# Optimization experiments

Hardware: AMD Instinct MI355X
Metric: run time of the kernel (lower is better)

## Reference

```python
import jax, jax.numpy as jnp
import numpy as np


def conv2d(x, w, b, pad):
    # x: NCHW, w: OIHW, stride 1, symmetric padding
    y = jax.lax.conv_general_dilated(
        x, w, window_strides=(1, 1), padding=[(pad, pad), (pad, pad)],
        dimension_numbers=('NCHW', 'OIHW', 'NCHW'))
    return y + b[None, :, None, None]


def setup_inputs() -> dict:
    key = jax.random.key(0)
    ks = jax.random.split(key, 10)
    N, Cin, H, W = 8, 256, 64, 64
    Cr = 64
    wscale = 0.02  # keep softmax logits moderate
    return {
        'feature_maps': jax.random.normal(ks[0], (N, Cin, H, W), jnp.float32),
        'global_channel_output': jax.random.normal(ks[1], (N, Cin, H, W), jnp.float32),
        'wq': jax.random.normal(ks[2], (Cr, Cin, 3, 3), jnp.float32) * wscale,
        'bq': jnp.zeros((Cr,), jnp.float32),
        'wk': jax.random.normal(ks[3], (Cr, Cin, 5, 5), jnp.float32) * wscale,
        'bk': jnp.zeros((Cr,), jnp.float32),
        'wv': jax.random.normal(ks[4], (Cr, Cin, 7, 7), jnp.float32) * wscale,
        'bv': jnp.zeros((Cr,), jnp.float32),
        'watt': jax.random.normal(ks[5], (Cin, Cr, 1, 1), jnp.float32) * wscale,
        'batt': jnp.zeros((Cin,), jnp.float32),
    }


def reference(feature_maps, global_channel_output, wq, bq, wk, bk, wv, bv, watt, batt):
    N, Cin, H, W = feature_maps.shape
    HW = H * W
    q = conv2d(feature_maps, wq, bq, 1).reshape(N, -1, HW)  # (N, Cr, HW)
    k = conv2d(feature_maps, wk, bk, 2).reshape(N, -1, HW)
    v = conv2d(feature_maps, wv, bv, 3).reshape(N, -1, HW)
    # key^T @ query: (N, HW, HW)
    qk = jnp.einsum('nci,ncj->nij', k, q)
    # GLOBAL softmax over the whole flattened HW*HW matrix per sample
    qk = jax.nn.softmax(qk.reshape(N, -1), axis=-1).reshape(N, HW, HW)
    att = jnp.einsum('nci,nij->ncj', v, qk).reshape(N, -1, H, W)  # (N, Cr, H, W)
    att = conv2d(att, watt, batt, 0)  # (N, Cin, H, W)
    return global_channel_output * att + global_channel_output
```

## Files before the change

### kernel.cpp

```cpp
#include <hip/hip_runtime.h>
#include <math.h>

#define NB 8
#define CIN 256
#define CR 64
#define H 64
#define W 64
#define HW 4096

typedef _Float16 f16;
typedef _Float16 f16x8 __attribute__((ext_vector_type(8)));
typedef _Float16 f16x4 __attribute__((ext_vector_type(4)));
typedef float f32x4 __attribute__((ext_vector_type(4)));

static const size_t QKV = (size_t)NB * CR * HW;

__global__ __launch_bounds__(256) void prep_w(
    const float* __restrict__ src, f16* __restrict__ dst, int KK)
{
    int idx = blockIdx.x * 256 + threadIdx.x;
    int ci = idx & 255;
    int co = (idx >> 8) & 63;
    int off = idx >> 14;
    dst[((size_t)(off * 64 + co)) * 256 + ci] = (f16)src[((size_t)(co * 256 + ci)) * KK + off];
}

__global__ __launch_bounds__(256) void transpose_fm(
    const float* __restrict__ fm, f16* __restrict__ fmT)
{
    const int y = blockIdx.x & 63;
    const int n = blockIdx.x >> 6;
    const int tid = threadIdx.x;
    __shared__ f16x4 tile[64 * 64];
    const int xw = tid & 63;
    const int wv = tid >> 6;
    const float* s0 = fm + ((size_t)n * CIN) * HW + y * W + xw;
#pragma unroll
    for (int cc = 0; cc < 16; ++cc) {
        const int slot = wv * 16 + cc;
        const float* s = s0 + (size_t)(slot * 4) * HW;
        f16x4 pk;
#pragma unroll
        for (int e = 0; e < 4; ++e) pk[e] = (f16)s[(size_t)e * HW];
        tile[xw * 64 + (slot ^ xw)] = pk;
    }
    __syncthreads();
    f16x4* dst = (f16x4*)fmT + ((size_t)n * HW + y * W) * 64;
#pragma unroll
    for (int it = 0; it < 16; ++it) {
        const int idx = tid + it * 256;
        const int x = idx >> 6;
        const int slot = idx & 63;
        dst[x * 64 + slot] = tile[x * 64 + (slot ^ x)];
    }
}

template<int K, int LAYOUT>
__global__ __launch_bounds__(512) void conv_mfma(
    const f16* __restrict__ fmT, const f16* __restrict__ wT,
    const float* __restrict__ bias, f16* __restrict__ dst)
{
    constexpr int P = K / 2;
    constexpr int XBYTES = 2 * 72 * 128;
    constexpr int WBYTES = K * 64 * 128;
    constexpr int TBYTES = XBYTES + WBYTES;
    constexpr int SBYTES = (TBYTES > 32768) ? TBYTES : 32768;
    __shared__ __align__(16) unsigned char smem[SBYTES];
    unsigned char* Xl = smem;
    unsigned char* Wl = smem + XBYTES;

    const int bid0 = blockIdx.x;
    const int bid = (bid0 & 7) * 32 + (bid0 >> 3);
    const int n  = bid >> 5;
    const int y0 = (bid & 31) * 2;
    const int tid = threadIdx.x;
    const int w = tid >> 6;
    const int lane = tid & 63;
    const int r  = w >> 2;
    const int h  = (w >> 1) & 1;
    const int sw = w & 1;
    const int lm = lane & 15;
    const int g  = lane >> 4;

    if (tid < 128) {
        const int sl = tid >> 6;
        const int cidx = (tid >> 3) & 7;
        const int chunk = tid & 7;
        const int col = (cidx < P) ? cidx : (64 + cidx);
        *(uint4*)(Xl + (size_t)(sl * 72 + col) * 128 + chunk * 16) = uint4{0, 0, 0, 0};
    }

    f32x4 acc[2][4];
#pragma unroll
    for (int i = 0; i < 2; ++i)
#pragma unroll
        for (int j = 0; j < 4; ++j) acc[i][j] = f32x4{0.f, 0.f, 0.f, 0.f};

    for (int dy = 0; dy < K; ++dy) {
        for (int ch = 0; ch < 4; ++ch) {
            __syncthreads();
#pragma unroll
            for (int p = 0; p < 2; ++p) {
                const int idx = tid + p * 512;
                const int sl = idx >> 9;
                const int x = (idx >> 3) & 63;
                const int chunk = idx & 7;
                const int iy = y0 + sl + dy - P;
                uint4 val = uint4{0, 0, 0, 0};
                if (iy >= 0 && iy < H)
                    val = *(const uint4*)(fmT + ((size_t)n * HW + iy * 64 + x) * 256 +
                                          ch * 64 + chunk * 8);
                *(uint4*)(Xl + (size_t)(sl * 72 + x + P) * 128 +
                          ((chunk * 16) ^ (((x + P) & 7) << 4))) = val;
            }
#pragma unroll
            for (int p = 0; p < K; ++p) {
                const int idx = tid + p * 512;
                const int cig = idx & 7;
                const int co  = (idx >> 3) & 63;
                const int dx  = idx >> 9;
                const f16* s = wT + ((size_t)((dy * K + dx) * 64 + co)) * 256 + ch * 64 + cig * 8;
                *(uint4*)(Wl + (size_t)(dx * 64 + co) * 128 +
                          ((cig * 16) ^ ((co & 7) << 4))) = *(const uint4*)s;
            }
            __syncthreads();
#pragma unroll
            for (int dx = 0; dx < K; ++dx) {
                f16x8 a[2], b[4];
#pragma unroll
                for (int cf = 0; cf < 2; ++cf) {
                    const int co = h * 32 + cf * 16 + lm;
                    a[cf] = *(const f16x8*)(Wl + (size_t)(dx * 64 + co) * 128 +
                                            ((sw * 64 + g * 16) ^ ((co & 7) << 4)));
                }
#pragma unroll
                for (int xf = 0; xf < 4; ++xf) {
                    const int col = xf * 16 + lm + dx;
                    b[xf] = *(const f16x8*)(Xl + (size_t)(r * 72 + col) * 128 +
                                            ((sw * 64 + g * 16) ^ ((col & 7) << 4)));
                }
#pragma unroll
                for (int cf = 0; cf < 2; ++cf)
#pragma unroll
                    for (int xf = 0; xf < 4; ++xf)
                        acc[cf][xf] = __builtin_amdgcn_mfma_f32_16x16x32_f16(
                            a[cf], b[xf], acc[cf][xf], 0, 0, 0);
            }
        }
    }

    __syncthreads();
    {
        const int mslot = r * 2 + h;
        if (sw == 1) {
#pragma unroll
            for (int cf = 0; cf < 2; ++cf)
#pragma unroll
                for (int xf = 0; xf < 4; ++xf)
                    *(f32x4*)(smem + (size_t)(mslot * 64 + lane) * 128 +
                              (((cf * 4 + xf) * 16) ^ ((lane & 7) << 4))) = acc[cf][xf];
        }
        __syncthreads();
        if (sw == 0) {
#pragma unroll
            for (int cf = 0; cf < 2; ++cf)
#pragma unroll
                for (int xf = 0; xf < 4; ++xf)
                    acc[cf][xf] += *(const f32x4*)(smem + (size_t)(mslot * 64 + lane) * 128 +
                                                   (((cf * 4 + xf) * 16) ^ ((lane & 7) << 4)));
        }
    }

    if (sw == 0) {
        const int y = y0 + r;
#pragma unroll
        for (int cf = 0; cf < 2; ++cf) {
            const float4 bv = *(const float4*)(bias + h * 32 + cf * 16 + g * 4);
            if (LAYOUT == 0) {
#pragma unroll
                for (int xf = 0; xf < 4; ++xf) {
                    f16x4 pk;
#pragma unroll
                    for (int e = 0; e < 4; ++e)
                        pk[e] = (f16)(acc[cf][xf][e] + ((const float*)&bv)[e]);
                    *(f16x4*)(dst + ((size_t)n * HW + y * W + xf * 16 + lm) * 64 +
                              h * 32 + cf * 16 + g * 4) = pk;
                }
            } else {
#pragma unroll
                for (int e = 0; e < 4; ++e) {
                    const int co = h * 32 + cf * 16 + g * 4 + e;
#pragma unroll
                    for (int xf = 0; xf < 4; ++xf)
                        dst[((size_t)(n * CR + co)) * HW + y * W + xf * 16 + lm] =
                            (f16)(acc[cf][xf][e] + ((const float*)&bv)[e]);
                }
            }
        }
    }
}

__global__ __launch_bounds__(256, 2) void attn_mfma(
    const f16* __restrict__ qT, const f16* __restrict__ kT, const f16* __restrict__ vv,
    f16* __restrict__ attu, float* __restrict__ Mcol, float* __restrict__ Zcol)
{
    const int bid0 = blockIdx.x;
    const int bid = (bid0 & 7) * 64 + (bid0 >> 3);
    const int jt = bid & 63;
    const int n  = bid >> 6;
    const int j0 = jt * 64;
    const int tid = threadIdx.x;
    const int wv = tid >> 6;
    const int lane = tid & 63;
    const int lm = lane & 15;
    const int g  = lane >> 4;
    const int key = (lm & 7) << 4;

    __shared__ __align__(16) f16 Qt[64 * 64];
    __shared__ __align__(16) f16 Kt[64 * 64];
    __shared__ __align__(16) f16 Vt[64 * 64];

    {
        const int r = tid >> 2;
        const f16* src = qT + ((size_t)n * HW + j0 + r) * 64;
#pragma unroll
        for (int h = 0; h < 2; ++h) {
            const int ch = (tid & 3) * 2 + h;
            *(uint4*)((char*)Qt + r * 128 + ((ch * 16) ^ ((r & 7) << 4))) =
                *(const uint4*)(src + ch * 8);
        }
    }

    float m = -1e30f, z = 0.f;
    f32x4 accp[4];
#pragma unroll
    for (int c = 0; c < 4; ++c) accp[c] = f32x4{0.f, 0.f, 0.f, 0.f};

    for (int it = 0; it < 64; ++it) {
        const int i0 = it * 64;
        __syncthreads();
        {
            const int r = tid >> 2;
            const f16* ks = kT + ((size_t)n * HW + i0 + r) * 64;
            const f16* vs = vv + ((size_t)n * CR + r) * HW + i0;
#pragma unroll
            for (int h = 0; h < 2; ++h) {
                const int ch = (tid & 3) * 2 + h;
                *(uint4*)((char*)Kt + r * 128 + ((ch * 16) ^ ((r & 7) << 4))) =
                    *(const uint4*)(ks + ch * 8);
                *(uint4*)((char*)Vt + r * 128 + ((ch * 16) ^ ((r & 7) << 4))) =
                    *(const uint4*)(vs + ch * 8);
            }
        }
        __syncthreads();

        f32x4 sacc[4];
#pragma unroll
        for (int f = 0; f < 4; ++f) sacc[f] = f32x4{0.f, 0.f, 0.f, 0.f};
#pragma unroll
        for (int ks = 0; ks < 2; ++ks) {
            const int off = (ks * 64 + g * 16);
            const f16x8 B = *(const f16x8*)((char*)Qt + (wv * 16 + lm) * 128 + (off ^ key));
#pragma unroll
            for (int f = 0; f < 4; ++f) {
                const f16x8 A = *(const f16x8*)((char*)Kt + (f * 16 + lm) * 128 + (off ^ key));
                sacc[f] = __builtin_amdgcn_mfma_f32_16x16x32_f16(A, B, sacc[f], 0, 0, 0);
            }
        }

        float mt = -1e30f;
#pragma unroll
        for (int f = 0; f < 4; ++f)
#pragma unroll
            for (int e = 0; e < 4; ++e) mt = fmaxf(mt, sacc[f][e]);
        mt = fmaxf(mt, __shfl_xor(mt, 16));
        mt = fmaxf(mt, __shfl_xor(mt, 32));
        const float mnew = fmaxf(m, mt);
        const float rr = __expf(m - mnew);
        m = mnew;

        f16x4 p16[4];
        float zt = 0.f;
#pragma unroll
        for (int f = 0; f < 4; ++f) {
#pragma unroll
            for (int e = 0; e < 4; ++e) {
                const float ev = __expf(sacc[f][e] - mnew);
                zt += ev;
                p16[f][e] = (f16)ev;
            }
        }
        zt += __shfl_xor(zt, 16);
        zt += __shfl_xor(zt, 32);
        z = z * rr + zt;

#pragma unroll
        for (int cf = 0; cf < 4; ++cf) {
            accp[cf][0] *= rr; accp[cf][1] *= rr;
            accp[cf][2] *= rr; accp[cf][3] *= rr;
        }

#pragma unroll
        for (int cf = 0; cf < 4; ++cf) {
#pragma unroll
            for (int f = 0; f < 4; ++f) {
                const f16x4 A = *(const f16x4*)((char*)Vt + (cf * 16 + lm) * 128 +
                                                ((f * 32 + g * 8) ^ key));
                accp[cf] = __builtin_amdgcn_mfma_f32_16x16x16f16(A, p16[f], accp[cf], 0, 0, 0);
            }
        }
    }

    const int j = j0 + wv * 16 + lm;
    const size_t jbase = ((size_t)n * HW + j) * 64;
#pragma unroll
    for (int cf = 0; cf < 4; ++cf) {
        f16x4 pk;
#pragma unroll
        for (int e = 0; e < 4; ++e) pk[e] = (f16)accp[cf][e];
        *(f16x4*)(attu + jbase + cf * 16 + g * 4) = pk;
    }
    if (g == 0) {
        Mcol[(size_t)n * HW + j] = m;
        Zcol[(size_t)n * HW + j] = z;
    }
}

__global__ __launch_bounds__(256) void reduce_kernel(
    const float* __restrict__ Mcol, const float* __restrict__ Zcol,
    float* __restrict__ Mn, float* __restrict__ Zn)
{
    const int n = blockIdx.x;
    const int tid = threadIdx.x;
    __shared__ float red[256];

    float lm = -1e30f;
    for (int j = tid; j < HW; j += 256) lm = fmaxf(lm, Mcol[(size_t)n * HW + j]);
    red[tid] = lm; __syncthreads();
    for (int s = 128; s > 0; s >>= 1) {
        if (tid < s) red[tid] = fmaxf(red[tid], red[tid + s]);
        __syncthreads();
    }
    const float M = red[0];
    __syncthreads();

    float ls = 0.f;
    for (int j = tid; j < HW; j += 256)
        ls += Zcol[(size_t)n * HW + j] * __expf(Mcol[(size_t)n * HW + j] - M);
    red[tid] = ls; __syncthreads();
    for (int s = 128; s > 0; s >>= 1) {
        if (tid < s) red[tid] += red[tid + s];
        __syncthreads();
    }
    if (tid == 0) { Mn[n] = M; Zn[n] = red[0]; }
}

__global__ __launch_bounds__(512) void final_mfma(
    const f16* __restrict__ attu, const float* __restrict__ Mcol,
    const float* __restrict__ Mn, const float* __restrict__ Zn,
    const float* __restrict__ watt, const float* __restrict__ batt,
    const float* __restrict__ gco, float* __restrict__ out)
{
    __shared__ __align__(16) f16 Wl[256 * 64];
    __shared__ __align__(16) f16 Al[128 * 64];

    const int bid0 = blockIdx.x;
    const int bid = (bid0 & 7) * 32 + (bid0 >> 3);
    const int n  = bid >> 5;
    const int p0 = (bid & 31) * 128;
    const int tid = threadIdx.x;
    const int wv = tid >> 6;
    const int lane = tid & 63;
    const int lm = lane & 15;
    const int g  = lane >> 4;

#pragma unroll
    for (int t = 0; t < 8; ++t) {
        const int idx = tid + t * 512;
        const int co = idx >> 4;
        const int ch = idx & 15;
        const float4 w4 = *(const float4*)(watt + (size_t)co * 64 + ch * 4);
        f16x4 pk;
        pk[0] = (f16)w4.x; pk[1] = (f16)w4.y; pk[2] = (f16)w4.z; pk[3] = (f16)w4.w;
        *(f16x4*)((char*)Wl + co * 128 + ((ch * 8) ^ ((co & 7) << 4))) = pk;
    }
#pragma unroll
    for (int t = 0; t < 4; ++t) {
        const int idx = tid + t * 512;
        const int pp = idx >> 3;
        const int ch = idx & 7;
        *(uint4*)((char*)Al + pp * 128 + ((ch * 16) ^ ((pp & 7) << 4))) =
            *(const uint4*)(attu + ((size_t)n * HW + p0 + pp) * 64 + ch * 8);
    }
    __syncthreads();

    f32x4 acc[2][8];
#pragma unroll
    for (int cf = 0; cf < 2; ++cf)
#pragma unroll
        for (int pf = 0; pf < 8; ++pf) acc[cf][pf] = f32x4{0.f, 0.f, 0.f, 0.f};

#pragma unroll
    for (int ks = 0; ks < 2; ++ks) {
        const int off = ks * 64 + g * 16;
        f16x8 A[2], B[8];
#pragma unroll
        for (int cf = 0; cf < 2; ++cf) {
            const int co = wv * 32 + cf * 16 + lm;
            A[cf] = *(const f16x8*)((char*)Wl + co * 128 + (off ^ ((co & 7) << 4)));
        }
#pragma unroll
        for (int pf = 0; pf < 8; ++pf) {
            const int pp = pf * 16 + lm;
            B[pf] = *(const f16x8*)((char*)Al + pp * 128 + (off ^ ((pp & 7) << 4)));
        }
#pragma unroll
        for (int cf = 0; cf < 2; ++cf)
#pragma unroll
            for (int pf = 0; pf < 8; ++pf)
                acc[cf][pf] = __builtin_amdgcn_mfma_f32_16x16x32_f16(
                    A[cf], B[pf], acc[cf][pf], 0, 0, 0);
    }

    const float M = Mn[n];
    const float Zi = 1.f / Zn[n];
    float ecol[8];
#pragma unroll
    for (int pf = 0; pf < 8; ++pf)
        ecol[pf] = __expf(Mcol[(size_t)n * HW + p0 + pf * 16 + lm] - M) * Zi;

#pragma unroll
    for (int cf = 0; cf < 2; ++cf) {
#pragma unroll
        for (int e = 0; e < 4; ++e) {
            const int co = wv * 32 + cf * 16 + g * 4 + e;
            const float bb = batt[co] + 1.f;
            const float* gsrc = gco + (size_t)(n * CIN + co) * HW + p0 + lm;
            float* dstp = out + (size_t)(n * CIN + co) * HW + p0 + lm;
#pragma unroll
            for (int pf = 0; pf < 8; ++pf) {
                const float gvv = gsrc[pf * 16];
                dstp[pf * 16] = gvv * (acc[cf][pf][e] * ecol[pf] + bb);
            }
        }
    }
}

extern "C" void kernel_launch(void* const* d_in, const int* in_sizes, int n_in,
                              void* d_out, int out_size, void* d_ws, size_t ws_size,
                              hipStream_t stream)
{
    (void)in_sizes; (void)n_in; (void)out_size; (void)ws_size;
    const float* fm   = (const float*)d_in[0];
    const float* gco  = (const float*)d_in[1];
    const float* wq   = (const float*)d_in[2];
    const float* bq   = (const float*)d_in[3];
    const float* wk   = (const float*)d_in[4];
    const float* bk   = (const float*)d_in[5];
    const float* wv   = (const float*)d_in[6];
    const float* bv   = (const float*)d_in[7];
    const float* watt = (const float*)d_in[8];
    const float* batt = (const float*)d_in[9];
    float* out = (float*)d_out;

    f16* qT   = (f16*)out;
    f16* kT   = qT + QKV;
    f16* vvb  = kT + QKV;
    f16* fmT  = vvb + QKV;

    unsigned char* wsb = (unsigned char*)d_ws;
    f16* wTq = (f16*)(wsb);
    f16* wTk = (f16*)(wsb + 294912);
    f16* wTv = (f16*)(wsb + 1114112);
    f16* attu = (f16*)(wsb + 2719744);
    float* Mcol = (float*)(wsb + 6914048);
    float* Zcol = (float*)(wsb + 7045120);
    float* Mn   = (float*)(wsb + 7176192);
    float* Zn   = (float*)(wsb + 7176224);

    prep_w<<<576, 256, 0, stream>>>(wq, wTq, 9);
    prep_w<<<1600, 256, 0, stream>>>(wk, wTk, 25);
    prep_w<<<3136, 256, 0, stream>>>(wv, wTv, 49);
    transpose_fm<<<NB * 64, 256, 0, stream>>>(fm, fmT);

    conv_mfma<3, 0><<<256, 512, 0, stream>>>(fmT, wTq, bq, qT);
    conv_mfma<5, 0><<<256, 512, 0, stream>>>(fmT, wTk, bk, kT);
    conv_mfma<7, 1><<<256, 512, 0, stream>>>(fmT, wTv, bv, vvb);

    attn_mfma<<<NB * 64, 256, 0, stream>>>(qT, kT, vvb, attu, Mcol, Zcol);
    reduce_kernel<<<NB, 256, 0, stream>>>(Mcol, Zcol, Mn, Zn);
    final_mfma<<<256, 512, 0, stream>>>(attu, Mcol, Mn, Zn, watt, batt, gco, out);
}
```

Baseline: 227.8 us.

## Rewrite attention kernel with 32x32 MFMA, register-resident Q, async LDS double buffering

```diff
diff --git a/kernel.cpp b/kernel.cpp
--- a/kernel.cpp
+++ b/kernel.cpp
@@ -12,8 +12,28 @@
 typedef _Float16 f16x8 __attribute__((ext_vector_type(8)));
 typedef _Float16 f16x4 __attribute__((ext_vector_type(4)));
 typedef float f32x4 __attribute__((ext_vector_type(4)));
+typedef float f32x16 __attribute__((ext_vector_type(16)));
+typedef unsigned int u32;
+typedef unsigned int u32x4 __attribute__((ext_vector_type(4)));
 
 static const size_t QKV = (size_t)NB * CR * HW;
+
+static __device__ __forceinline__ void gl_lds16(const f16* g, f16* l) {
+    __builtin_amdgcn_global_load_lds(
+        (const __attribute__((address_space(1))) void*)g,
+        (__attribute__((address_space(3))) void*)l, 16, 0, 0);
+}
+
+static __device__ __forceinline__ u32 pk2(float a, float b) {
+    return __builtin_bit_cast(u32, __builtin_amdgcn_cvt_pkrtz(a, b));
+}
+
+static __device__ __forceinline__ f32x16 zero16() {
+    f32x16 v;
+#pragma unroll
+    for (int i = 0; i < 16; ++i) v[i] = 0.f;
+    return v;
+}
 
 __global__ __launch_bounds__(256) void prep_w(
     const float* __restrict__ src, f16* __restrict__ dst, int KK)
@@ -58,7 +78,7 @@
 template<int K, int LAYOUT>
 __global__ __launch_bounds__(512) void conv_mfma(
     const f16* __restrict__ fmT, const f16* __restrict__ wT,
-    const float* __restrict__ bias, f16* __restrict__ dst)
+    const float* __restrict__ bias, f16* __restrict__ dst, float oscale)
 {
     constexpr int P = K / 2;
     constexpr int XBYTES = 2 * 72 * 128;
@@ -182,7 +202,7 @@
                     f16x4 pk;
 #pragma unroll
                     for (int e = 0; e < 4; ++e)
-                        pk[e] = (f16)(acc[cf][xf][e] + ((const float*)&bv)[e]);
+                        pk[e] = (f16)((acc[cf][xf][e] + ((const float*)&bv)[e]) * oscale);
                     *(f16x4*)(dst + ((size_t)n * HW + y * W + xf * 16 + lm) * 64 +
                               h * 32 + cf * 16 + g * 4) = pk;
                 }
@@ -193,134 +213,159 @@
 #pragma unroll
                     for (int xf = 0; xf < 4; ++xf)
                         dst[((size_t)(n * CR + co)) * HW + y * W + xf * 16 + lm] =
-                            (f16)(acc[cf][xf][e] + ((const float*)&bv)[e]);
+                            (f16)((acc[cf][xf][e] + ((const float*)&bv)[e]) * oscale);
                 }
             }
         }
     }
 }
 
-__global__ __launch_bounds__(256, 2) void attn_mfma(
+__global__ __launch_bounds__(256, 1) void attn_mfma(
     const f16* __restrict__ qT, const f16* __restrict__ kT, const f16* __restrict__ vv,
     f16* __restrict__ attu, float* __restrict__ Mcol, float* __restrict__ Zcol)
 {
     const int bid0 = blockIdx.x;
-    const int bid = (bid0 & 7) * 64 + (bid0 >> 3);
-    const int jt = bid & 63;
-    const int n  = bid >> 6;
-    const int j0 = jt * 64;
+    const int bid = (bid0 & 7) * 32 + (bid0 >> 3);
+    const int n  = bid >> 5;
+    const int jb = bid & 31;
     const int tid = threadIdx.x;
     const int wv = tid >> 6;
     const int lane = tid & 63;
-    const int lm = lane & 15;
-    const int g  = lane >> 4;
-    const int key = (lm & 7) << 4;
-
-    __shared__ __align__(16) f16 Qt[64 * 64];
-    __shared__ __align__(16) f16 Kt[64 * 64];
-    __shared__ __align__(16) f16 Vt[64 * 64];
-
+    const int lm5 = lane & 31;
+    const int g1 = lane >> 5;
+    const int j = jb * 128 + wv * 32 + lm5;
+    const int key = (lm5 & 7) << 4;
+
+    __shared__ __align__(16) f16 KV[2][2][64 * 64];
+
+    const int rsub = lane >> 3;
+    const int perm = ((lane & 7) ^ rsub) << 3;
+    const f16* kS = kT + ((size_t)n * HW) * 64;
+    const f16* vS = vv + ((size_t)n * CR) * HW;
+
+    f16x8 qf[4];
     {
-        const int r = tid >> 2;
-        const f16* src = qT + ((size_t)n * HW + j0 + r) * 64;
-#pragma unroll
-        for (int h = 0; h < 2; ++h) {
-            const int ch = (tid & 3) * 2 + h;
-            *(uint4*)((char*)Qt + r * 128 + ((ch * 16) ^ ((r & 7) << 4))) =
-                *(const uint4*)(src + ch * 8);
-        }
+        const f16* qp = qT + ((size_t)n * HW + j) * 64 + g1 * 8;
+#pragma unroll
+        for (int ks = 0; ks < 4; ++ks) qf[ks] = *(const f16x8*)(qp + ks * 16);
     }
 
     float m = -1e30f, z = 0.f;
-    f32x4 accp[4];
-#pragma unroll
-    for (int c = 0; c < 4; ++c) accp[c] = f32x4{0.f, 0.f, 0.f, 0.f};
-
+    f32x16 acc0 = zero16(), acc1 = zero16();
+
+#pragma unroll
+    for (int h = 0; h < 2; ++h) {
+        const int q = 2 * wv + h;
+        gl_lds16(kS + (size_t)(q * 8 + rsub) * 64 + perm, &KV[0][0][q * 512]);
+        gl_lds16(vS + (size_t)(q * 8 + rsub) * HW + perm, &KV[0][1][q * 512]);
+    }
+    __syncthreads();
+
+    int buf = 0;
     for (int it = 0; it < 64; ++it) {
-        const int i0 = it * 64;
-        __syncthreads();
-        {
-            const int r = tid >> 2;
-            const f16* ks = kT + ((size_t)n * HW + i0 + r) * 64;
-            const f16* vs = vv + ((size_t)n * CR + r) * HW + i0;
+        const char* Kb = (const char*)&KV[buf][0][0];
+        f32x16 s0 = zero16(), s1 = zero16();
+        __builtin_amdgcn_s_setprio(1);
+#pragma unroll
+        for (int ks = 0; ks < 4; ++ks) {
+            const int off = ((ks * 32 + g1 * 16) ^ key);
+            const f16x8 A0 = *(const f16x8*)(Kb + lm5 * 128 + off);
+            const f16x8 A1 = *(const f16x8*)(Kb + (32 + lm5) * 128 + off);
+            s0 = __builtin_amdgcn_mfma_f32_32x32x16_f16(A0, qf[ks], s0, 0, 0, 0);
+            s1 = __builtin_amdgcn_mfma_f32_32x32x16_f16(A1, qf[ks], s1, 0, 0, 0);
+        }
+        __builtin_amdgcn_s_setprio(0);
+
+        if (it < 63) {
 #pragma unroll
             for (int h = 0; h < 2; ++h) {
-                const int ch = (tid & 3) * 2 + h;
-                *(uint4*)((char*)Kt + r * 128 + ((ch * 16) ^ ((r & 7) << 4))) =
-                    *(const uint4*)(ks + ch * 8);
-                *(uint4*)((char*)Vt + r * 128 + ((ch * 16) ^ ((r & 7) << 4))) =
-                    *(const uint4*)(vs + ch * 8);
-            }
-        }
-        __syncthreads();
-
-        f32x4 sacc[4];
-#pragma unroll
-        for (int f = 0; f < 4; ++f) sacc[f] = f32x4{0.f, 0.f, 0.f, 0.f};
-#pragma unroll
-        for (int ks = 0; ks < 2; ++ks) {
-            const int off = (ks * 64 + g * 16);
-            const f16x8 B = *(const f16x8*)((char*)Qt + (wv * 16 + lm) * 128 + (off ^ key));
-#pragma unroll
-            for (int f = 0; f < 4; ++f) {
-                const f16x8 A = *(const f16x8*)((char*)Kt + (f * 16 + lm) * 128 + (off ^ key));
-                sacc[f] = __builtin_amdgcn_mfma_f32_16x16x32_f16(A, B, sacc[f], 0, 0, 0);
-            }
-        }
-
-        float mt = -1e30f;
-#pragma unroll
-        for (int f = 0; f < 4; ++f)
-#pragma unroll
-            for (int e = 0; e < 4; ++e) mt = fmaxf(mt, sacc[f][e]);
-        mt = fmaxf(mt, __shfl_xor(mt, 16));
+                const int q = 2 * wv + h;
+                gl_lds16(kS + (size_t)((it + 1) * 64 + q * 8 + rsub) * 64 + perm,
+                         &KV[buf ^ 1][0][q * 512]);
+                gl_lds16(vS + (size_t)(q * 8 + rsub) * HW + (it + 1) * 64 + perm,
+                         &KV[buf ^ 1][1][q * 512]);
+            }
+        }
+
+        float mt = s0[0];
+#pragma unroll
+        for (int rr2 = 1; rr2 < 16; ++rr2) mt = fmaxf(mt, s0[rr2]);
+#pragma unroll
+        for (int rr2 = 0; rr2 < 16; ++rr2) mt = fmaxf(mt, s1[rr2]);
         mt = fmaxf(mt, __shfl_xor(mt, 32));
-        const float mnew = fmaxf(m, mt);
-        const float rr = __expf(m - mnew);
-        m = mnew;
-
-        f16x4 p16[4];
+        if (__ballot(mt > m)) {
+            const float mnew = fmaxf(m, mt);
+            const float rsc = exp2f(m - mnew);
+            z *= rsc;
+#pragma unroll
+            for (int rr2 = 0; rr2 < 16; ++rr2) { acc0[rr2] *= rsc; acc1[rr2] *= rsc; }
+            m = mnew;
+        }
         float zt = 0.f;
-#pragma unroll
-        for (int f = 0; f < 4; ++f) {
-#pragma unroll
-            for (int e = 0; e < 4; ++e) {
-                const float ev = __expf(sacc[f][e] - mnew);
-                zt += ev;
-                p16[f][e] = (f16)ev;
-            }
-        }
-        zt += __shfl_xor(zt, 16);
+        u32 pa0[8], pa1[8];
+#pragma unroll
+        for (int a = 0; a < 4; ++a) {
+            float p0 = exp2f(s0[4 * a + 0] - m), p1 = exp2f(s0[4 * a + 1] - m);
+            float p2 = exp2f(s0[4 * a + 2] - m), p3 = exp2f(s0[4 * a + 3] - m);
+            zt += (p0 + p1) + (p2 + p3);
+            pa0[a * 2 + 0] = pk2(p0, p1); pa0[a * 2 + 1] = pk2(p2, p3);
+            float q0 = exp2f(s1[4 * a + 0] - m), q1 = exp2f(s1[4 * a + 1] - m);
+            float q2 = exp2f(s1[4 * a + 2] - m), q3 = exp2f(s1[4 * a + 3] - m);
+            zt += (q0 + q1) + (q2 + q3);
+            pa1[a * 2 + 0] = pk2(q0, q1); pa1[a * 2 + 1] = pk2(q2, q3);
+        }
         zt += __shfl_xor(zt, 32);
-        z = z * rr + zt;
-
-#pragma unroll
-        for (int cf = 0; cf < 4; ++cf) {
-            accp[cf][0] *= rr; accp[cf][1] *= rr;
-            accp[cf][2] *= rr; accp[cf][3] *= rr;
-        }
-
-#pragma unroll
-        for (int cf = 0; cf < 4; ++cf) {
-#pragma unroll
-            for (int f = 0; f < 4; ++f) {
-                const f16x4 A = *(const f16x4*)((char*)Vt + (cf * 16 + lm) * 128 +
-                                                ((f * 32 + g * 8) ^ key));
-                accp[cf] = __builtin_amdgcn_mfma_f32_16x16x16f16(A, p16[f], accp[cf], 0, 0, 0);
-            }
-        }
-    }
-
-    const int j = j0 + wv * 16 + lm;
+        z += zt;
+
+        u32 bfu[4][4];
+#pragma unroll
+        for (int it2 = 0; it2 < 2; ++it2) {
+            const u32* P = (it2 == 0) ? pa0 : pa1;
+#pragma unroll
+            for (int k2 = 0; k2 < 2; ++k2) {
+                const u32 sA = g1 ? P[(k2 * 2 + 0) * 2 + 0] : P[(k2 * 2 + 1) * 2 + 0];
+                const u32 sB = g1 ? P[(k2 * 2 + 0) * 2 + 1] : P[(k2 * 2 + 1) * 2 + 1];
+                const u32 rA = __shfl_xor(sA, 32);
+                const u32 rB = __shfl_xor(sB, 32);
+                const u32 oA = g1 ? P[(k2 * 2 + 1) * 2 + 0] : P[(k2 * 2 + 0) * 2 + 0];
+                const u32 oB = g1 ? P[(k2 * 2 + 1) * 2 + 1] : P[(k2 * 2 + 0) * 2 + 1];
+                bfu[it2 * 2 + k2][0] = g1 ? rA : oA;
+                bfu[it2 * 2 + k2][1] = g1 ? rB : oB;
+                bfu[it2 * 2 + k2][2] = g1 ? oA : rA;
+                bfu[it2 * 2 + k2][3] = g1 ? oB : rB;
+            }
+        }
+
+        const char* Vb = (const char*)&KV[buf][1][0];
+        __builtin_amdgcn_s_setprio(1);
+#pragma unroll
+        for (int ks2 = 0; ks2 < 4; ++ks2) {
+            const f16x8 B = __builtin_bit_cast(
+                f16x8, (u32x4){bfu[ks2][0], bfu[ks2][1], bfu[ks2][2], bfu[ks2][3]});
+            const int off = ((ks2 * 32 + g1 * 16) ^ key);
+            const f16x8 A0 = *(const f16x8*)(Vb + lm5 * 128 + off);
+            const f16x8 A1 = *(const f16x8*)(Vb + (32 + lm5) * 128 + off);
+            acc0 = __builtin_amdgcn_mfma_f32_32x32x16_f16(A0, B, acc0, 0, 0, 0);
+            acc1 = __builtin_amdgcn_mfma_f32_32x32x16_f16(A1, B, acc1, 0, 0, 0);
+        }
+        __builtin_amdgcn_s_setprio(0);
+
+        if (it < 63) {
+            __syncthreads();
+            buf ^= 1;
+        }
+    }
+
     const size_t jbase = ((size_t)n * HW + j) * 64;
 #pragma unroll
-    for (int cf = 0; cf < 4; ++cf) {
-        f16x4 pk;
-#pragma unroll
-        for (int e = 0; e < 4; ++e) pk[e] = (f16)accp[cf][e];
-        *(f16x4*)(attu + jbase + cf * 16 + g * 4) = pk;
-    }
-    if (g == 0) {
+    for (int a = 0; a < 4; ++a) {
+        f16x4 pk0, pk1;
+#pragma unroll
+        for (int e = 0; e < 4; ++e) { pk0[e] = (f16)acc0[4 * a + e]; pk1[e] = (f16)acc1[4 * a + e]; }
+        *(f16x4*)(attu + jbase + a * 8 + g1 * 4) = pk0;
+        *(f16x4*)(attu + jbase + 32 + a * 8 + g1 * 4) = pk1;
+    }
+    if (g1 == 0) {
         Mcol[(size_t)n * HW + j] = m;
         Zcol[(size_t)n * HW + j] = z;
     }
@@ -346,7 +391,7 @@
 
     float ls = 0.f;
     for (int j = tid; j < HW; j += 256)
-        ls += Zcol[(size_t)n * HW + j] * __expf(Mcol[(size_t)n * HW + j] - M);
+        ls += Zcol[(size_t)n * HW + j] * exp2f(Mcol[(size_t)n * HW + j] - M);
     red[tid] = ls; __syncthreads();
     for (int s = 128; s > 0; s >>= 1) {
         if (tid < s) red[tid] += red[tid + s];
@@ -427,7 +472,7 @@
     float ecol[8];
 #pragma unroll
     for (int pf = 0; pf < 8; ++pf)
-        ecol[pf] = __expf(Mcol[(size_t)n * HW + p0 + pf * 16 + lm] - M) * Zi;
+        ecol[pf] = exp2f(Mcol[(size_t)n * HW + p0 + pf * 16 + lm] - M) * Zi;
 
 #pragma unroll
     for (int cf = 0; cf < 2; ++cf) {
@@ -478,16 +523,18 @@
     float* Mn   = (float*)(wsb + 7176192);
     float* Zn   = (float*)(wsb + 7176224);
 
+    const float LOG2E = 1.4426950408889634f;
+
     prep_w<<<576, 256, 0, stream>>>(wq, wTq, 9);
     prep_w<<<1600, 256, 0, stream>>>(wk, wTk, 25);
     prep_w<<<3136, 256, 0, stream>>>(wv, wTv, 49);
     transpose_fm<<<NB * 64, 256, 0, stream>>>(fm, fmT);
 
-    conv_mfma<3, 0><<<256, 512, 0, stream>>>(fmT, wTq, bq, qT);
-    conv_mfma<5, 0><<<256, 512, 0, stream>>>(fmT, wTk, bk, kT);
-    conv_mfma<7, 1><<<256, 512, 0, stream>>>(fmT, wTv, bv, vvb);
-
-    attn_mfma<<<NB * 64, 256, 0, stream>>>(qT, kT, vvb, attu, Mcol, Zcol);
+    conv_mfma<3, 0><<<256, 512, 0, stream>>>(fmT, wTq, bq, qT, LOG2E);
+    conv_mfma<5, 0><<<256, 512, 0, stream>>>(fmT, wTk, bk, kT, 1.0f);
+    conv_mfma<7, 1><<<256, 512, 0, stream>>>(fmT, wTv, bv, vvb, 1.0f);
+
+    attn_mfma<<<256, 256, 0, stream>>>(qT, kT, vvb, attu, Mcol, Zcol);
     reduce_kernel<<<NB, 256, 0, stream>>>(Mcol, Zcol, Mn, Zn);
     final_mfma<<<256, 512, 0, stream>>>(attu, Mcol, Mn, Zn, watt, batt, gco, out);
 }
```

Measured after the change: 253.9 us. 11.5% more time.

## Double-buffer K/V via direct global-to-LDS loads and use exp2 with prescaled Q

Applied to the files above, without the earlier changes.

```diff
diff --git a/kernel.cpp b/kernel.cpp
--- a/kernel.cpp
+++ b/kernel.cpp
@@ -14,6 +14,12 @@
 typedef float f32x4 __attribute__((ext_vector_type(4)));
 
 static const size_t QKV = (size_t)NB * CR * HW;
+
+static __device__ __forceinline__ void gl_lds16(const f16* g, f16* l) {
+    __builtin_amdgcn_global_load_lds(
+        (const __attribute__((address_space(1))) void*)g,
+        (__attribute__((address_space(3))) void*)l, 16, 0, 0);
+}
 
 __global__ __launch_bounds__(256) void prep_w(
     const float* __restrict__ src, f16* __restrict__ dst, int KK)
@@ -58,7 +64,7 @@
 template<int K, int LAYOUT>
 __global__ __launch_bounds__(512) void conv_mfma(
     const f16* __restrict__ fmT, const f16* __restrict__ wT,
-    const float* __restrict__ bias, f16* __restrict__ dst)
+    const float* __restrict__ bias, f16* __restrict__ dst, float oscale)
 {
     constexpr int P = K / 2;
     constexpr int XBYTES = 2 * 72 * 128;
@@ -94,7 +100,7 @@
 #pragma unroll
     for (int i = 0; i < 2; ++i)
 #pragma unroll
-        for (int j = 0; j < 4; ++j) acc[i][j] = f32x4{0.f, 0.f, 0.f, 0.f};
+        for (int jx = 0; jx < 4; ++jx) acc[i][jx] = f32x4{0.f, 0.f, 0.f, 0.f};
 
     for (int dy = 0; dy < K; ++dy) {
         for (int ch = 0; ch < 4; ++ch) {
@@ -182,7 +188,7 @@
                     f16x4 pk;
 #pragma unroll
                     for (int e = 0; e < 4; ++e)
-                        pk[e] = (f16)(acc[cf][xf][e] + ((const float*)&bv)[e]);
+                        pk[e] = (f16)((acc[cf][xf][e] + ((const float*)&bv)[e]) * oscale);
                     *(f16x4*)(dst + ((size_t)n * HW + y * W + xf * 16 + lm) * 64 +
                               h * 32 + cf * 16 + g * 4) = pk;
                 }
@@ -193,7 +199,7 @@
 #pragma unroll
                     for (int xf = 0; xf < 4; ++xf)
                         dst[((size_t)(n * CR + co)) * HW + y * W + xf * 16 + lm] =
-                            (f16)(acc[cf][xf][e] + ((const float*)&bv)[e]);
+                            (f16)((acc[cf][xf][e] + ((const float*)&bv)[e]) * oscale);
                 }
             }
         }
@@ -215,20 +221,20 @@
     const int lm = lane & 15;
     const int g  = lane >> 4;
     const int key = (lm & 7) << 4;
-
-    __shared__ __align__(16) f16 Qt[64 * 64];
-    __shared__ __align__(16) f16 Kt[64 * 64];
-    __shared__ __align__(16) f16 Vt[64 * 64];
-
+    const int j = j0 + wv * 16 + lm;
+
+    __shared__ __align__(16) f16 KV[2][2][64 * 64];
+
+    const int rsub = lane >> 3;
+    const int perm = ((lane & 7) ^ rsub) << 3;
+    const f16* kS = kT + ((size_t)n * HW) * 64;
+    const f16* vS = vv + ((size_t)n * CR) * HW;
+
+    f16x8 qf[2];
     {
-        const int r = tid >> 2;
-        const f16* src = qT + ((size_t)n * HW + j0 + r) * 64;
-#pragma unroll
-        for (int h = 0; h < 2; ++h) {
-            const int ch = (tid & 3) * 2 + h;
-            *(uint4*)((char*)Qt + r * 128 + ((ch * 16) ^ ((r & 7) << 4))) =
-                *(const uint4*)(src + ch * 8);
-        }
+        const f16* qp = qT + ((size_t)n * HW + j) * 64 + g * 8;
+        qf[0] = *(const f16x8*)(qp);
+        qf[1] = *(const f16x8*)(qp + 32);
     }
 
     float m = -1e30f, z = 0.f;
@@ -236,82 +242,95 @@
 #pragma unroll
     for (int c = 0; c < 4; ++c) accp[c] = f32x4{0.f, 0.f, 0.f, 0.f};
 
+#pragma unroll
+    for (int h = 0; h < 2; ++h) {
+        const int q = 2 * wv + h;
+        gl_lds16(kS + (size_t)(q * 8 + rsub) * 64 + perm, &KV[0][0][q * 512]);
+        gl_lds16(vS + (size_t)(q * 8 + rsub) * HW + perm, &KV[0][1][q * 512]);
+    }
+    __syncthreads();
+
+    int buf = 0;
     for (int it = 0; it < 64; ++it) {
-        const int i0 = it * 64;
-        __syncthreads();
-        {
-            const int r = tid >> 2;
-            const f16* ks = kT + ((size_t)n * HW + i0 + r) * 64;
-            const f16* vs = vv + ((size_t)n * CR + r) * HW + i0;
+        if (it < 63) {
 #pragma unroll
             for (int h = 0; h < 2; ++h) {
-                const int ch = (tid & 3) * 2 + h;
-                *(uint4*)((char*)Kt + r * 128 + ((ch * 16) ^ ((r & 7) << 4))) =
-                    *(const uint4*)(ks + ch * 8);
-                *(uint4*)((char*)Vt + r * 128 + ((ch * 16) ^ ((r & 7) << 4))) =
-                    *(const uint4*)(vs + ch * 8);
-            }
-        }
-        __syncthreads();
-
+                const int q = 2 * wv + h;
+                gl_lds16(kS + (size_t)((it + 1) * 64 + q * 8 + rsub) * 64 + perm,
+                         &KV[buf ^ 1][0][q * 512]);
+                gl_lds16(vS + (size_t)(q * 8 + rsub) * HW + (it + 1) * 64 + perm,
+                         &KV[buf ^ 1][1][q * 512]);
+            }
+        }
+
+        const char* Kb = (const char*)&KV[buf][0][0];
         f32x4 sacc[4];
 #pragma unroll
         for (int f = 0; f < 4; ++f) sacc[f] = f32x4{0.f, 0.f, 0.f, 0.f};
+        __builtin_amdgcn_s_setprio(1);
 #pragma unroll
         for (int ks = 0; ks < 2; ++ks) {
-            const int off = (ks * 64 + g * 16);
-            const f16x8 B = *(const f16x8*)((char*)Qt + (wv * 16 + lm) * 128 + (off ^ key));
+            const int off = (ks * 64 + g * 16) ^ key;
 #pragma unroll
             for (int f = 0; f < 4; ++f) {
-                const f16x8 A = *(const f16x8*)((char*)Kt + (f * 16 + lm) * 128 + (off ^ key));
-                sacc[f] = __builtin_amdgcn_mfma_f32_16x16x32_f16(A, B, sacc[f], 0, 0, 0);
-            }
-        }
-
-        float mt = -1e30f;
+                const f16x8 A = *(const f16x8*)(Kb + (f * 16 + lm) * 128 + off);
+                sacc[f] = __builtin_amdgcn_mfma_f32_16x16x32_f16(A, qf[ks], sacc[f], 0, 0, 0);
+            }
+        }
+        __builtin_amdgcn_s_setprio(0);
+
+        float mt = sacc[0][0];
 #pragma unroll
         for (int f = 0; f < 4; ++f)
 #pragma unroll
             for (int e = 0; e < 4; ++e) mt = fmaxf(mt, sacc[f][e]);
         mt = fmaxf(mt, __shfl_xor(mt, 16));
         mt = fmaxf(mt, __shfl_xor(mt, 32));
-        const float mnew = fmaxf(m, mt);
-        const float rr = __expf(m - mnew);
-        m = mnew;
-
+        if (__ballot(mt > m)) {
+            const float mnew = fmaxf(m, mt);
+            const float rsc = exp2f(m - mnew);
+            z *= rsc;
+#pragma unroll
+            for (int cf = 0; cf < 4; ++cf) {
+                accp[cf][0] *= rsc; accp[cf][1] *= rsc;
+                accp[cf][2] *= rsc; accp[cf][3] *= rsc;
+            }
+            m = mnew;
+        }
         f16x4 p16[4];
         float zt = 0.f;
 #pragma unroll
         for (int f = 0; f < 4; ++f) {
 #pragma unroll
             for (int e = 0; e < 4; ++e) {
-                const float ev = __expf(sacc[f][e] - mnew);
+                const float ev = exp2f(sacc[f][e] - m);
                 zt += ev;
                 p16[f][e] = (f16)ev;
             }
         }
         zt += __shfl_xor(zt, 16);
         zt += __shfl_xor(zt, 32);
-        z = z * rr + zt;
-
+        z += zt;
+
+        const char* Vb = (const char*)&KV[buf][1][0];
+        __builtin_amdgcn_s_setprio(1);
 #pragma unroll
         for (int cf = 0; cf < 4; ++cf) {
-            accp[cf][0] *= rr; accp[cf][1] *= rr;
-            accp[cf][2] *= rr; accp[cf][3] *= rr;
-        }
-
-#pragma unroll
-        for (int cf = 0; cf < 4; ++cf) {
 #pragma unroll
             for (int f = 0; f < 4; ++f) {
-                const f16x4 A = *(const f16x4*)((char*)Vt + (cf * 16 + lm) * 128 +
+                const f16x4 A = *(const f16x4*)(Vb + (cf * 16 + lm) * 128 +
                                                 ((f * 32 + g * 8) ^ key));
                 accp[cf] = __builtin_amdgcn_mfma_f32_16x16x16f16(A, p16[f], accp[cf], 0, 0, 0);
             }
         }
-    }
-
-    const int j = j0 + wv * 16 + lm;
+        __builtin_amdgcn_s_setprio(0);
+
+        if (it < 63) {
+            __syncthreads();
+            buf ^= 1;
+        }
+    }
+
     const size_t jbase = ((size_t)n * HW + j) * 64;
 #pragma unroll
     for (int cf = 0; cf < 4; ++cf) {
@@ -346,7 +365,7 @@
 
     float ls = 0.f;
     for (int j = tid; j < HW; j += 256)
-        ls += Zcol[(size_t)n * HW + j] * __expf(Mcol[(size_t)n * HW + j] - M);
+        ls += Zcol[(size_t)n * HW + j] * exp2f(Mcol[(size_t)n * HW + j] - M);
     red[tid] = ls; __syncthreads();
     for (int s = 128; s > 0; s >>= 1) {
         if (tid < s) red[tid] += red[tid + s];
@@ -427,7 +446,7 @@
     float ecol[8];
 #pragma unroll
     for (int pf = 0; pf < 8; ++pf)
-        ecol[pf] = __expf(Mcol[(size_t)n * HW + p0 + pf * 16 + lm] - M) * Zi;
+        ecol[pf] = exp2f(Mcol[(size_t)n * HW + p0 + pf * 16 + lm] - M) * Zi;
 
 #pragma unroll
     for (int cf = 0; cf < 2; ++cf) {
@@ -478,14 +497,16 @@
     float* Mn   = (float*)(wsb + 7176192);
     float* Zn   = (float*)(wsb + 7176224);
 
+    const float LOG2E = 1.4426950408889634f;
+
     prep_w<<<576, 256, 0, stream>>>(wq, wTq, 9);
     prep_w<<<1600, 256, 0, stream>>>(wk, wTk, 25);
     prep_w<<<3136, 256, 0, stream>>>(wv, wTv, 49);
     transpose_fm<<<NB * 64, 256, 0, stream>>>(fm, fmT);
 
-    conv_mfma<3, 0><<<256, 512, 0, stream>>>(fmT, wTq, bq, qT);
-    conv_mfma<5, 0><<<256, 512, 0, stream>>>(fmT, wTk, bk, kT);
-    conv_mfma<7, 1><<<256, 512, 0, stream>>>(fmT, wTv, bv, vvb);
+    conv_mfma<3, 0><<<256, 512, 0, stream>>>(fmT, wTq, bq, qT, LOG2E);
+    conv_mfma<5, 0><<<256, 512, 0, stream>>>(fmT, wTk, bk, kT, 1.0f);
+    conv_mfma<7, 1><<<256, 512, 0, stream>>>(fmT, wTv, bv, vvb, 1.0f);
 
     attn_mfma<<<NB * 64, 256, 0, stream>>>(qT, kT, vvb, attu, Mcol, Zcol);
     reduce_kernel<<<NB, 256, 0, stream>>>(Mcol, Zcol, Mn, Zn);
```

Measured after the change: 239.6 us. 1.05x slower.

## Merge conv and weight-prep launches, fold log2e into Q, and skip unneeded rescales

Applied to the files above, without the earlier changes.

```diff
diff --git a/kernel.cpp b/kernel.cpp
--- a/kernel.cpp
+++ b/kernel.cpp
@@ -15,10 +15,21 @@
 
 static const size_t QKV = (size_t)NB * CR * HW;
 
-__global__ __launch_bounds__(256) void prep_w(
-    const float* __restrict__ src, f16* __restrict__ dst, int KK)
-{
-    int idx = blockIdx.x * 256 + threadIdx.x;
+static __device__ __forceinline__ float ex2(float x) {
+    return __builtin_amdgcn_exp2f(x);
+}
+
+__global__ __launch_bounds__(256) void prep_all(
+    const float* __restrict__ wq, const float* __restrict__ wk,
+    const float* __restrict__ wv,
+    f16* __restrict__ dq, f16* __restrict__ dk, f16* __restrict__ dv)
+{
+    int b = blockIdx.x;
+    const float* src; f16* dst; int KK;
+    if (b < 576)       { src = wq; dst = dq; KK = 9; }
+    else if (b < 2176) { src = wk; dst = dk; KK = 25; b -= 576; }
+    else               { src = wv; dst = dv; KK = 49; b -= 2176; }
+    int idx = b * 256 + threadIdx.x;
     int ci = idx & 255;
     int co = (idx >> 8) & 63;
     int off = idx >> 14;
@@ -56,20 +67,16 @@
 }
 
 template<int K, int LAYOUT>
-__global__ __launch_bounds__(512) void conv_mfma(
+static __device__ __forceinline__ void conv_body(
     const f16* __restrict__ fmT, const f16* __restrict__ wT,
-    const float* __restrict__ bias, f16* __restrict__ dst)
+    const float* __restrict__ bias, f16* __restrict__ dst, float oscale,
+    unsigned char* smem, int bid0)
 {
     constexpr int P = K / 2;
     constexpr int XBYTES = 2 * 72 * 128;
-    constexpr int WBYTES = K * 64 * 128;
-    constexpr int TBYTES = XBYTES + WBYTES;
-    constexpr int SBYTES = (TBYTES > 32768) ? TBYTES : 32768;
-    __shared__ __align__(16) unsigned char smem[SBYTES];
     unsigned char* Xl = smem;
     unsigned char* Wl = smem + XBYTES;
 
-    const int bid0 = blockIdx.x;
     const int bid = (bid0 & 7) * 32 + (bid0 >> 3);
     const int n  = bid >> 5;
     const int y0 = (bid & 31) * 2;
@@ -94,7 +101,7 @@
 #pragma unroll
     for (int i = 0; i < 2; ++i)
 #pragma unroll
-        for (int j = 0; j < 4; ++j) acc[i][j] = f32x4{0.f, 0.f, 0.f, 0.f};
+        for (int jx = 0; jx < 4; ++jx) acc[i][jx] = f32x4{0.f, 0.f, 0.f, 0.f};
 
     for (int dy = 0; dy < K; ++dy) {
         for (int ch = 0; ch < 4; ++ch) {
@@ -182,7 +189,7 @@
                     f16x4 pk;
 #pragma unroll
                     for (int e = 0; e < 4; ++e)
-                        pk[e] = (f16)(acc[cf][xf][e] + ((const float*)&bv)[e]);
+                        pk[e] = (f16)((acc[cf][xf][e] + ((const float*)&bv)[e]) * oscale);
                     *(f16x4*)(dst + ((size_t)n * HW + y * W + xf * 16 + lm) * 64 +
                               h * 32 + cf * 16 + g * 4) = pk;
                 }
@@ -193,11 +200,24 @@
 #pragma unroll
                     for (int xf = 0; xf < 4; ++xf)
                         dst[((size_t)(n * CR + co)) * HW + y * W + xf * 16 + lm] =
-                            (f16)(acc[cf][xf][e] + ((const float*)&bv)[e]);
+                            (f16)((acc[cf][xf][e] + ((const float*)&bv)[e]) * oscale);
                 }
             }
         }
     }
+}
+
+__global__ __launch_bounds__(512) void conv_all(
+    const f16* __restrict__ fmT,
+    const f16* __restrict__ wTq, const f16* __restrict__ wTk, const f16* __restrict__ wTv,
+    const float* __restrict__ bq, const float* __restrict__ bk, const float* __restrict__ bv,
+    f16* __restrict__ qT, f16* __restrict__ kT, f16* __restrict__ vvb, float log2e)
+{
+    __shared__ __align__(16) unsigned char smem[2 * 72 * 128 + 7 * 64 * 128];
+    const int b = blockIdx.x;
+    if (b < 256)      conv_body<3, 0>(fmT, wTq, bq, qT, log2e, smem, b);
+    else if (b < 512) conv_body<5, 0>(fmT, wTk, bk, kT, 1.0f, smem, b - 256);
+    else              conv_body<7, 1>(fmT, wTv, bv, vvb, 1.0f, smem, b - 512);
 }
 
 __global__ __launch_bounds__(256, 2) void attn_mfma(
@@ -258,8 +278,8 @@
 #pragma unroll
         for (int f = 0; f < 4; ++f) sacc[f] = f32x4{0.f, 0.f, 0.f, 0.f};
 #pragma unroll
-        for (int ks = 0; ks < 2; ++ks) {
-            const int off = (ks * 64 + g * 16);
+        for (int ks2 = 0; ks2 < 2; ++ks2) {
+            const int off = (ks2 * 64 + g * 16);
             const f16x8 B = *(const f16x8*)((char*)Qt + (wv * 16 + lm) * 128 + (off ^ key));
 #pragma unroll
             for (int f = 0; f < 4; ++f) {
@@ -268,37 +288,38 @@
             }
         }
 
-        float mt = -1e30f;
-#pragma unroll
-        for (int f = 0; f < 4; ++f)
-#pragma unroll
-            for (int e = 0; e < 4; ++e) mt = fmaxf(mt, sacc[f][e]);
+        const float mA = fmaxf(fmaxf(sacc[0][0], sacc[0][1]), fmaxf(sacc[0][2], sacc[0][3]));
+        const float mB = fmaxf(fmaxf(sacc[1][0], sacc[1][1]), fmaxf(sacc[1][2], sacc[1][3]));
+        const float mC = fmaxf(fmaxf(sacc[2][0], sacc[2][1]), fmaxf(sacc[2][2], sacc[2][3]));
+        const float mD = fmaxf(fmaxf(sacc[3][0], sacc[3][1]), fmaxf(sacc[3][2], sacc[3][3]));
+        float mt = fmaxf(fmaxf(mA, mB), fmaxf(mC, mD));
         mt = fmaxf(mt, __shfl_xor(mt, 16));
         mt = fmaxf(mt, __shfl_xor(mt, 32));
-        const float mnew = fmaxf(m, mt);
-        const float rr = __expf(m - mnew);
-        m = mnew;
-
+        if (__ballot(mt > m)) {
+            const float mnew = fmaxf(m, mt);
+            const float rsc = ex2(m - mnew);
+            z *= rsc;
+#pragma unroll
+            for (int cf = 0; cf < 4; ++cf) {
+                accp[cf][0] *= rsc; accp[cf][1] *= rsc;
+                accp[cf][2] *= rsc; accp[cf][3] *= rsc;
+            }
+            m = mnew;
+        }
         f16x4 p16[4];
-        float zt = 0.f;
+        float zp[4];
 #pragma unroll
         for (int f = 0; f < 4; ++f) {
-#pragma unroll
-            for (int e = 0; e < 4; ++e) {
-                const float ev = __expf(sacc[f][e] - mnew);
-                zt += ev;
-                p16[f][e] = (f16)ev;
-            }
-        }
+            const float e0 = ex2(sacc[f][0] - m), e1 = ex2(sacc[f][1] - m);
+            const float e2 = ex2(sacc[f][2] - m), e3 = ex2(sacc[f][3] - m);
+            zp[f] = (e0 + e1) + (e2 + e3);
+            p16[f][0] = (f16)e0; p16[f][1] = (f16)e1;
+            p16[f][2] = (f16)e2; p16[f][3] = (f16)e3;
+        }
+        float zt = (zp[0] + zp[1]) + (zp[2] + zp[3]);
         zt += __shfl_xor(zt, 16);
         zt += __shfl_xor(zt, 32);
-        z = z * rr + zt;
-
-#pragma unroll
-        for (int cf = 0; cf < 4; ++cf) {
-            accp[cf][0] *= rr; accp[cf][1] *= rr;
-            accp[cf][2] *= rr; accp[cf][3] *= rr;
-        }
+        z += zt;
 
 #pragma unroll
         for (int cf = 0; cf < 4; ++cf) {
@@ -346,7 +367,7 @@
 
     float ls = 0.f;
     for (int j = tid; j < HW; j += 256)
-        ls += Zcol[(size_t)n * HW + j] * __expf(Mcol[(size_t)n * HW + j] - M);
+        ls += Zcol[(size_t)n * HW + j] * ex2(Mcol[(size_t)n * HW + j] - M);
     red[tid] = ls; __syncthreads();
     for (int s = 128; s > 0; s >>= 1) {
         if (tid < s) red[tid] += red[tid + s];
@@ -427,7 +448,7 @@
     float ecol[8];
 #pragma unroll
     for (int pf = 0; pf < 8; ++pf)
-        ecol[pf] = __expf(Mcol[(size_t)n * HW + p0 + pf * 16 + lm] - M) * Zi;
+        ecol[pf] = ex2(Mcol[(size_t)n * HW + p0 + pf * 16 + lm] - M) * Zi;
 
 #pragma unroll
     for (int cf = 0; cf < 2; ++cf) {
@@ -478,14 +499,13 @@
     float* Mn   = (float*)(wsb + 7176192);
     float* Zn   = (float*)(wsb + 7176224);
 
-    prep_w<<<576, 256, 0, stream>>>(wq, wTq, 9);
-    prep_w<<<1600, 256, 0, stream>>>(wk, wTk, 25);
-    prep_w<<<3136, 256, 0, stream>>>(wv, wTv, 49);
+    const float LOG2E = 1.4426950408889634f;
+
+    prep_all<<<5312, 256, 0, stream>>>(wq, wk, wv, wTq, wTk, wTv);
     transpose_fm<<<NB * 64, 256, 0, stream>>>(fm, fmT);
 
-    conv_mfma<3, 0><<<256, 512, 0, stream>>>(fmT, wTq, bq, qT);
-    conv_mfma<5, 0><<<256, 512, 0, stream>>>(fmT, wTk, bk, kT);
-    conv_mfma<7, 1><<<256, 512, 0, stream>>>(fmT, wTv, bv, vvb);
+    conv_all<<<768, 512, 0, stream>>>(fmT, wTq, wTk, wTv, bq, bk, bv,
+                                      qT, kT, vvb, LOG2E);
 
     attn_mfma<<<NB * 64, 256, 0, stream>>>(qT, kT, vvb, attu, Mcol, Zcol);
     reduce_kernel<<<NB, 256, 0, stream>>>(Mcol, Zcol, Mn, Zn);
```

Measured after the change: 220.9 us. 1.03x faster.
